# Kernel optimization log

Hardware: AMD Instinct MI355X
Metric: run time of the kernel (lower is better)

Reference implementation:

```python
import jax, jax.numpy as jnp
import numpy as np

N = 100000      # num graph nodes
E = 1600000     # num edges (avg degree 16)
IN = 128        # in_channels
H = 128         # hidden_channels
B = 4096        # query batch
CTX = 20        # context set length (indices[:, 3:])


def setup_inputs() -> dict:
    key = jax.random.key(0)
    ks = jax.random.split(key, 16)
    inp = {
        "indices": jax.random.randint(ks[0], (B, 3 + CTX), 0, N, dtype=jnp.int64),
        "src": jax.random.randint(ks[1], (E,), 0, N, dtype=jnp.int32),
        "dst": jax.random.randint(ks[2], (E,), 0, N, dtype=jnp.int32),
        "w": jax.random.uniform(ks[3], (E,), dtype=jnp.float32),
        # learned params
        "ndata": jax.random.normal(ks[4], (N, IN), dtype=jnp.float32),
        "W1": jax.random.normal(ks[5], (H, IN), dtype=jnp.float32) * (1.0 / np.sqrt(IN)),
        "b1": jnp.zeros((H,), jnp.float32),
        "W2": jax.random.normal(ks[6], (H, H), dtype=jnp.float32) * (1.0 / np.sqrt(H)),
        "b2": jnp.zeros((H,), jnp.float32),
        "eps": jnp.zeros((2,), jnp.float32),  # learn_eps, one per GINConv
        "Wc1": jax.random.normal(ks[7], (H, 3 * H), dtype=jnp.float32) * (1.0 / np.sqrt(3 * H)),
        "bc1": jnp.zeros((H,), jnp.float32),
        "Wc2": jax.random.normal(ks[8], (H // 2, H), dtype=jnp.float32) * (1.0 / np.sqrt(H)),
        "bc2": jnp.zeros((H // 2,), jnp.float32),
        "Wc3": jax.random.normal(ks[9], (1, H // 2), dtype=jnp.float32) * (1.0 / np.sqrt(H // 2)),
        "bc3": jnp.zeros((1,), jnp.float32),
    }
    return inp


def _gin_conv(x, src, dst, w, deg, eps, W, b):
    # DGL GINConv(mean, learn_eps): h = lin((1+eps)*x + mean_{in-edges}(w_e * x_src))
    msg = w[:, None] * x[src]                                   # [E, D]
    agg = jax.ops.segment_sum(msg, dst, num_segments=N) / deg   # [N, D]
    return ((1.0 + eps) * x + agg) @ W.T + b


def reference(indices, src, dst, w, ndata, W1, b1, W2, b2, eps,
              Wc1, bc1, Wc2, bc2, Wc3, bc3):
    deg = jax.ops.segment_sum(jnp.ones((E,), ndata.dtype), dst, num_segments=N)
    deg = jnp.maximum(deg, 1.0)[:, None]

    x = ndata
    x = jax.nn.relu(_gin_conv(x, src, dst, w, deg, eps[0], W1, b1))  # dropout inactive (eval)
    x = _gin_conv(x, src, dst, w, deg, eps[1], W2, b2)               # last layer: no relu
    x = x.at[0].set(0.0)                                             # x[0] = zeros

    ing1 = x[indices[:, 0]]   # [B, H]
    ing2 = x[indices[:, 1]]   # [B, H]

    # embed_context: mean over nonzero-index context members
    ctx_idx = indices[:, 3:]                                   # [B, CTX]
    ctx_sum = x[ctx_idx].sum(axis=1)                           # [B, H]
    norm = jnp.maximum((ctx_idx > 0).sum(axis=1), 1).astype(x.dtype)[:, None]
    ctx = ctx_sum / norm

    y = jnp.concatenate([ing1, ing2, ctx], axis=1)             # [B, 3H]
    y = jax.nn.relu(y @ Wc1.T + bc1)
    y = jax.nn.relu(y @ Wc2.T + bc2)
    y = y @ Wc3.T + bc3                                        # [B, 1]
    return y
```

## Files before the change

kernel.cpp:

```cpp
#include <hip/hip_runtime.h>


#define CONV_NPB 32
#define FIN_EPB 8

__global__ void init_kernel(const float* __restrict__ W1, const float* __restrict__ W2,
                            const float* __restrict__ Wc1, const float* __restrict__ Wc2,
                            float* __restrict__ Wt1, float* __restrict__ Wt2,
                            float* __restrict__ Wc1t, float* __restrict__ Wc2t,
                            int* __restrict__ cnt, int n) {
  int i = blockIdx.x * blockDim.x + threadIdx.x;
  if (i < n) cnt[i] = 0;
  if (i < 16384) {
    int f = i >> 7, k = i & 127;
    Wt1[k * 128 + f] = W1[i];
  } else if (i < 32768) {
    int j = i - 16384; int f = j >> 7, k = j & 127;
    Wt2[k * 128 + f] = W2[j];
  } else if (i < 81920) {
    int j = i - 32768; int f = j / 384, k = j % 384;
    Wc1t[k * 128 + f] = Wc1[j];
  } else if (i < 90112) {
    int j = i - 81920; int f = j >> 7, k = j & 127;
    Wc2t[k * 64 + f] = Wc2[j];
  }
}

__global__ void hist_kernel(const int* __restrict__ dst, int* __restrict__ cnt,
                            int* __restrict__ rank, int E) {
  int e = (blockIdx.x * blockDim.x + threadIdx.x) * 4;
  if (e + 3 < E) {
    const int4 d = *(const int4*)&dst[e];
    int4 r;
    r.x = atomicAdd(&cnt[d.x], 1);
    r.y = atomicAdd(&cnt[d.y], 1);
    r.z = atomicAdd(&cnt[d.z], 1);
    r.w = atomicAdd(&cnt[d.w], 1);
    *(int4*)&rank[e] = r;
  } else {
    for (; e < E; ++e) rank[e] = atomicAdd(&cnt[dst[e]], 1);
  }
}

__global__ void scan1_kernel(const int* __restrict__ cnt, int* __restrict__ prow,
                             int* __restrict__ bsum, int n) {
  __shared__ int smem[256];
  const int t = threadIdx.x;
  const int base = blockIdx.x * 2048 + t * 8;
  int v[8];
  int s = 0;
#pragma unroll
  for (int j = 0; j < 8; ++j) {
    int idx = base + j;
    v[j] = (idx < n) ? ((cnt[idx] + 7) & ~7) : 0;
    s += v[j];
  }
  smem[t] = s;
  __syncthreads();
  for (int off = 1; off < 256; off <<= 1) {
    int add = (t >= off) ? smem[t - off] : 0;
    __syncthreads();
    smem[t] += add;
    __syncthreads();
  }
  int run = smem[t] - s;
  if (t == 255) bsum[blockIdx.x] = smem[255];
#pragma unroll
  for (int j = 0; j < 8; ++j) {
    int idx = base + j;
    if (idx < n) prow[idx] = run;
    run += v[j];
  }
}

__global__ void scan2_kernel(int* __restrict__ bsum, int nb) {
  const int t = threadIdx.x;
  if (nb <= 64) {
    const int orig = (t < nb) ? bsum[t] : 0;
    int v = orig;
#pragma unroll
    for (int off = 1; off < 64; off <<= 1) {
      int u = __shfl_up(v, off);
      if (t >= off) v += u;
    }
    if (t == nb - 1) bsum[nb] = v;
    if (t < nb) bsum[t] = v - orig;
  } else if (t == 0) {
    int run = 0;
    for (int i = 0; i < nb; ++i) { int v = bsum[i]; bsum[i] = run; run += v; }
    bsum[nb] = run;
  }
}

__global__ void scatter_kernel(const int* __restrict__ src, const int* __restrict__ dst,
                               const float* __restrict__ w, const int* __restrict__ prow,
                               const int* __restrict__ bsum, const int* __restrict__ rank,
                               const int* __restrict__ cnt,
                               int2* __restrict__ epack, int E, int n) {
  const int i = blockIdx.x * blockDim.x + threadIdx.x;
  int e = i * 4;
  if (e + 3 < E) {
    const int4 d = *(const int4*)&dst[e];
    const int4 s = *(const int4*)&src[e];
    const float4 wv = *(const float4*)&w[e];
    const int4 r = *(const int4*)&rank[e];
    epack[prow[d.x] + bsum[d.x >> 11] + r.x] = make_int2(s.x, __float_as_int(wv.x));
    epack[prow[d.y] + bsum[d.y >> 11] + r.y] = make_int2(s.y, __float_as_int(wv.y));
    epack[prow[d.z] + bsum[d.z >> 11] + r.z] = make_int2(s.z, __float_as_int(wv.z));
    epack[prow[d.w] + bsum[d.w >> 11] + r.w] = make_int2(s.w, __float_as_int(wv.w));
  } else {
    for (; e < E; ++e) {
      const int d = dst[e];
      epack[prow[d] + bsum[d >> 11] + rank[e]] = make_int2(src[e], __float_as_int(w[e]));
    }
  }
  if (i < n) {
    const int c = cnt[i];
    const int start = prow[i] + bsum[i >> 11] + c;
    const int pc = ((c + 7) & ~7) - c;
    for (int j = 0; j < pc; ++j) epack[start + j] = make_int2(0, 0);
  }
}

__launch_bounds__(256, 6)
__global__ void conv_kernel(const float* __restrict__ xin, float* __restrict__ xout,
                            const int* __restrict__ prow, const int* __restrict__ bsum,
                            const int* __restrict__ cnt,
                            const int2* __restrict__ epack,
                            const float* __restrict__ Wt,
                            const float* __restrict__ bias, const float* __restrict__ eps,
                            int epsidx, int dorelu, int zerorow0, int n, int nchunk) {
  __shared__ float xm[CONV_NPB * 128];
  __shared__ int rp_s[CONV_NPB + 1];
  const int t = threadIdx.x;
  const int nb = blockIdx.x * CONV_NPB;
  const float epsv = 1.0f + eps[epsidx];

#pragma unroll
  for (int i = 0; i < 4; ++i)
    *(float4*)&xm[(t + i * 256) * 4] = make_float4(0.f, 0.f, 0.f, 0.f);
  if (t <= CONV_NPB) {
    const int node = nb + t;
    rp_s[t] = (node >= n) ? bsum[nchunk] : (prow[node] + bsum[node >> 11]);
  }
  __syncthreads();

  {
    const int L = t >> 5;
    const int lane = t & 31;
    const int f0 = lane * 4;
    const int e0 = rp_s[0], eT = rp_s[CONV_NPB];
    const int nbat = (eT - e0) >> 3;
    const int chunk = (((nbat + 7) >> 3)) << 3;
    const int jb = e0 + L * chunk;
    const int je = min(jb + chunk, eT);
    if (jb < je) {
      const int4* ep4 = (const int4*)epack;
      int r = 0;
      while (rp_s[r + 1] <= jb) ++r;
      float4 acc = make_float4(0.f, 0.f, 0.f, 0.f);
      for (int j = jb; j < je; j += 8) {
        if (rp_s[r + 1] <= j) {
          float* bp = &xm[r * 128 + lane];
          atomicAdd(bp + 0,  acc.x);
          atomicAdd(bp + 32, acc.y);
          atomicAdd(bp + 64, acc.z);
          atomicAdd(bp + 96, acc.w);
          acc = make_float4(0.f, 0.f, 0.f, 0.f);
          do { ++r; } while (rp_s[r + 1] <= j);
        }
        const int h = j >> 1;
        const int4 q0 = ep4[h + 0];
        const int4 q1 = ep4[h + 1];
        const int4 q2 = ep4[h + 2];
        const int4 q3 = ep4[h + 3];
        const float4 a0 = *(const float4*)&xin[(size_t)q0.x * 128 + f0];
        const float4 a1 = *(const float4*)&xin[(size_t)q0.z * 128 + f0];
        const float4 a2 = *(const float4*)&xin[(size_t)q1.x * 128 + f0];
        const float4 a3 = *(const float4*)&xin[(size_t)q1.z * 128 + f0];
        const float4 a4 = *(const float4*)&xin[(size_t)q2.x * 128 + f0];
        const float4 a5 = *(const float4*)&xin[(size_t)q2.z * 128 + f0];
        const float4 a6 = *(const float4*)&xin[(size_t)q3.x * 128 + f0];
        const float4 a7 = *(const float4*)&xin[(size_t)q3.z * 128 + f0];
        const float w0 = __int_as_float(q0.y), w1 = __int_as_float(q0.w);
        const float w2 = __int_as_float(q1.y), w3 = __int_as_float(q1.w);
        const float w4 = __int_as_float(q2.y), w5 = __int_as_float(q2.w);
        const float w6 = __int_as_float(q3.y), w7 = __int_as_float(q3.w);
        acc.x += w0 * a0.x + w1 * a1.x + w2 * a2.x + w3 * a3.x
               + w4 * a4.x + w5 * a5.x + w6 * a6.x + w7 * a7.x;
        acc.y += w0 * a0.y + w1 * a1.y + w2 * a2.y + w3 * a3.y
               + w4 * a4.y + w5 * a5.y + w6 * a6.y + w7 * a7.y;
        acc.z += w0 * a0.z + w1 * a1.z + w2 * a2.z + w3 * a3.z
               + w4 * a4.z + w5 * a5.z + w6 * a6.z + w7 * a7.z;
        acc.w += w0 * a0.w + w1 * a1.w + w2 * a2.w + w3 * a3.w
               + w4 * a4.w + w5 * a5.w + w6 * a6.w + w7 * a7.w;
      }
      float* bp = &xm[r * 128 + lane];
      atomicAdd(bp + 0,  acc.x);
      atomicAdd(bp + 32, acc.y);
      atomicAdd(bp + 64, acc.z);
      atomicAdd(bp + 96, acc.w);
    }
  }
  __syncthreads();

  {
    float4 m[4];
#pragma unroll
    for (int q = 0; q < 4; ++q) {
      const int task = t + q * 256;
      const int r = task >> 5;
      const int fg = task & 31;
      m[q].x = xm[r * 128 + fg];
      m[q].y = xm[r * 128 + 32 + fg];
      m[q].z = xm[r * 128 + 64 + fg];
      m[q].w = xm[r * 128 + 96 + fg];
    }
    __syncthreads();
#pragma unroll
    for (int q = 0; q < 4; ++q) {
      const int task = t + q * 256;
      const int r = task >> 5;
      const int fg = task & 31;
      const int f0 = fg * 4;
      const int node = nb + r;
      float4 v = make_float4(0.f, 0.f, 0.f, 0.f);
      if (node < n) {
        const int d = cnt[node];
        const float rdeg = 1.0f / (float)(d > 1 ? d : 1);
        const float4 xv = *(const float4*)&xin[(size_t)node * 128 + f0];
        v.x = epsv * xv.x + m[q].x * rdeg;
        v.y = epsv * xv.y + m[q].y * rdeg;
        v.z = epsv * xv.z + m[q].z * rdeg;
        v.w = epsv * xv.w + m[q].w * rdeg;
      }
      *(float4*)&xm[r * 128 + f0] = v;
    }
  }
  __syncthreads();

  {
    const int fg = t & 31;
    const int rg = t >> 5;
    const int f0 = fg * 4;
    const int r0 = rg * 4;
    float4 acc[4];
#pragma unroll
    for (int r = 0; r < 4; ++r) acc[r] = make_float4(0.f, 0.f, 0.f, 0.f);
    for (int k = 0; k < 128; k += 4) {
      const float4 w0 = *(const float4*)&Wt[(k + 0) * 128 + f0];
      const float4 w1 = *(const float4*)&Wt[(k + 1) * 128 + f0];
      const float4 w2 = *(const float4*)&Wt[(k + 2) * 128 + f0];
      const float4 w3 = *(const float4*)&Wt[(k + 3) * 128 + f0];
#pragma unroll
      for (int r = 0; r < 4; ++r) {
        const float4 xv = *(const float4*)&xm[(r0 + r) * 128 + k];
        acc[r].x += xv.x * w0.x + xv.y * w1.x + xv.z * w2.x + xv.w * w3.x;
        acc[r].y += xv.x * w0.y + xv.y * w1.y + xv.z * w2.y + xv.w * w3.y;
        acc[r].z += xv.x * w0.z + xv.y * w1.z + xv.z * w2.z + xv.w * w3.z;
        acc[r].w += xv.x * w0.w + xv.y * w1.w + xv.z * w2.w + xv.w * w3.w;
      }
    }
    const float4 bv = *(const float4*)&bias[f0];
#pragma unroll
    for (int r = 0; r < 4; ++r) {
      const int node = nb + r0 + r;
      if (node < n) {
        float4 v;
        v.x = acc[r].x + bv.x;
        v.y = acc[r].y + bv.y;
        v.z = acc[r].z + bv.z;
        v.w = acc[r].w + bv.w;
        if (dorelu) {
          v.x = fmaxf(v.x, 0.f); v.y = fmaxf(v.y, 0.f);
          v.z = fmaxf(v.z, 0.f); v.w = fmaxf(v.w, 0.f);
        }
        if (zerorow0 && node == 0) { v.x = 0.f; v.y = 0.f; v.z = 0.f; v.w = 0.f; }
        *(float4*)&xout[(size_t)node * 128 + f0] = v;
      }
    }
  }
}

__launch_bounds__(256, 4)
__global__ void final_kernel(const float* __restrict__ x2, const int* __restrict__ indices,
                             const float* __restrict__ Wc1t, const float* __restrict__ bc1,
                             const float* __restrict__ Wc2t, const float* __restrict__ bc2,
                             const float* __restrict__ Wc3, const float* __restrict__ bc3,
                             float* __restrict__ out) {
  __shared__ float ysm[FIN_EPB * 384];
  __shared__ float h1s[FIN_EPB * 128];
  __shared__ float h2s[FIN_EPB * 64];
  __shared__ int ind_s[FIN_EPB * 23];
  __shared__ float ccs[FIN_EPB];
  const int t = threadIdx.x;
  const int b0 = blockIdx.x * FIN_EPB;

  if (t < FIN_EPB * 23) ind_s[t] = indices[(size_t)b0 * 23 + t];
  __syncthreads();
  if (t < FIN_EPB) {
    int cc = 0;
#pragma unroll
    for (int j = 0; j < 20; ++j) cc += (ind_s[t * 23 + 3 + j] > 0) ? 1 : 0;
    ccs[t] = 1.0f / (float)(cc > 0 ? cc : 1);
  }
  __syncthreads();

  {
#pragma unroll
    for (int q = 0; q < 2; ++q) {
      const int s = t + q * 256;
      const int e = s >> 6;
      const int half = (s >> 5) & 1;
      const int fg = s & 31;
      const int idx = ind_s[e * 23 + half];
      *(float4*)&ysm[e * 384 + half * 128 + fg * 4] =
          *(const float4*)&x2[(size_t)idx * 128 + fg * 4];
    }
    const int e = t >> 5;
    const int fg = t & 31;
    float4 acc = make_float4(0.f, 0.f, 0.f, 0.f);
#pragma unroll
    for (int j = 0; j < 20; ++j) {
      const int cj = ind_s[e * 23 + 3 + j];
      const float4 a = *(const float4*)&x2[(size_t)cj * 128 + fg * 4];
      acc.x += a.x; acc.y += a.y; acc.z += a.z; acc.w += a.w;
    }
    const float sc = ccs[e];
    acc.x *= sc; acc.y *= sc; acc.z *= sc; acc.w *= sc;
    *(float4*)&ysm[e * 384 + 256 + fg * 4] = acc;
  }
  __syncthreads();

  {
    const int f1 = t & 127;
    const int eh = t >> 7;
    float acc[4];
    const float b = bc1[f1];
#pragma unroll
    for (int i = 0; i < 4; ++i) acc[i] = b;
    for (int k = 0; k < 384; k += 4) {
      const float wv0 = Wc1t[(k + 0) * 128 + f1];
      const float wv1 = Wc1t[(k + 1) * 128 + f1];
      const float wv2 = Wc1t[(k + 2) * 128 + f1];
      const float wv3 = Wc1t[(k + 3) * 128 + f1];
#pragma unroll
      for (int i = 0; i < 4; ++i) {
        const float4 yv = *(const float4*)&ysm[(eh * 4 + i) * 384 + k];
        acc[i] += yv.x * wv0 + yv.y * wv1 + yv.z * wv2 + yv.w * wv3;
      }
    }
#pragma unroll
    for (int i = 0; i < 4; ++i)
      h1s[(eh * 4 + i) * 128 + f1] = fmaxf(acc[i], 0.f);
  }
  __syncthreads();

  {
    const int f2 = t & 63;
    const int eg = t >> 6;
    float acc[2];
    const float b = bc2[f2];
#pragma unroll
    for (int i = 0; i < 2; ++i) acc[i] = b;
    for (int k = 0; k < 128; k += 4) {
      const float wv0 = Wc2t[(k + 0) * 64 + f2];
      const float wv1 = Wc2t[(k + 1) * 64 + f2];
      const float wv2 = Wc2t[(k + 2) * 64 + f2];
      const float wv3 = Wc2t[(k + 3) * 64 + f2];
#pragma unroll
      for (int i = 0; i < 2; ++i) {
        const float4 hv = *(const float4*)&h1s[(eg * 2 + i) * 128 + k];
        acc[i] += hv.x * wv0 + hv.y * wv1 + hv.z * wv2 + hv.w * wv3;
      }
    }
#pragma unroll
    for (int i = 0; i < 2; ++i)
      h2s[(eg * 2 + i) * 64 + f2] = fmaxf(acc[i], 0.f);
  }
  __syncthreads();

  {
    const int e = t >> 5;
    const int l = t & 31;
    float p = h2s[e * 64 + l] * Wc3[l] + h2s[e * 64 + l + 32] * Wc3[l + 32];
#pragma unroll
    for (int o = 16; o > 0; o >>= 1) p += __shfl_down(p, o, 32);
    if (l == 0) out[b0 + e] = p + bc3[0];
  }
}

extern "C" void kernel_launch(void* const* d_in, const int* in_sizes, int n_in,
                              void* d_out, int out_size, void* d_ws, size_t ws_size,
                              hipStream_t stream) {
  const int* indices = (const int*)d_in[0];
  const int* src = (const int*)d_in[1];
  const int* dst = (const int*)d_in[2];
  const float* w = (const float*)d_in[3];
  const float* ndata = (const float*)d_in[4];
  const float* W1 = (const float*)d_in[5];
  const float* b1 = (const float*)d_in[6];
  const float* W2 = (const float*)d_in[7];
  const float* b2 = (const float*)d_in[8];
  const float* eps = (const float*)d_in[9];
  const float* Wc1 = (const float*)d_in[10];
  const float* bc1 = (const float*)d_in[11];
  const float* Wc2 = (const float*)d_in[12];
  const float* bc2 = (const float*)d_in[13];
  const float* Wc3 = (const float*)d_in[14];
  const float* bc3 = (const float*)d_in[15];
  float* out = (float*)d_out;

  const int E = in_sizes[1];
  const int N = in_sizes[4] / 128;
  const int B = in_sizes[0] / 23;

  char* ws = (char*)d_ws;
  size_t off = 0;
  auto alloc = [&](size_t bytes) -> char* {
    char* p = ws + off;
    off = (off + bytes + 255) & ~(size_t)255;
    return p;
  };
  const size_t Epad = (size_t)E + 8 * (size_t)N;
  int* cnt = (int*)alloc((size_t)N * 4);
  int* prow = (int*)alloc((size_t)(N + 1) * 4);
  int* rank = (int*)alloc((size_t)E * 4);
  int* bsum = (int*)alloc(256 * 4);
  int2* epack = (int2*)alloc(Epad * 8);
  float* x1 = (float*)alloc((size_t)N * 128 * 4);
  float* x2 = (float*)alloc((size_t)N * 128 * 4);
  float* Wt1 = (float*)alloc(16384 * 4);
  float* Wt2 = (float*)alloc(16384 * 4);
  float* Wc1t = (float*)alloc(49152 * 4);
  float* Wc2t = (float*)alloc(8192 * 4);

  const int ninit = (N > 90112) ? N : 90112;
  init_kernel<<<(ninit + 255) / 256, 256, 0, stream>>>(W1, W2, Wc1, Wc2, Wt1, Wt2, Wc1t, Wc2t, cnt, N);
  const int Eq = (E + 3) / 4;
  hist_kernel<<<(Eq + 255) / 256, 256, 0, stream>>>(dst, cnt, rank, E);
  const int nchunk = (N + 2047) / 2048;
  scan1_kernel<<<nchunk, 256, 0, stream>>>(cnt, prow, bsum, N);
  scan2_kernel<<<1, 64, 0, stream>>>(bsum, nchunk);
  const int nsc = (Eq > N) ? Eq : N;
  scatter_kernel<<<(nsc + 255) / 256, 256, 0, stream>>>(src, dst, w, prow, bsum, rank, cnt, epack, E, N);

  const int nconv = (N + CONV_NPB - 1) / CONV_NPB;
  conv_kernel<<<nconv, 256, 0, stream>>>(ndata, x1, prow, bsum, cnt, epack, Wt1, b1, eps, 0, 1, 0, N, nchunk);
  conv_kernel<<<nconv, 256, 0, stream>>>(x1, x2, prow, bsum, cnt, epack, Wt2, b2, eps, 1, 0, 1, N, nchunk);

  final_kernel<<<B / FIN_EPB, 256, 0, stream>>>(x2, indices, Wc1t, bc1, Wc2t, bc2, Wc3, bc3, out);
}
```

Before: 593.0 us.

## Split fused conv into feature-sliced aggregation kernel and separate GEMM kernel

```diff
diff --git a/kernel.cpp b/kernel.cpp
--- a/kernel.cpp
+++ b/kernel.cpp
@@ -122,23 +122,22 @@
   }
 }
 
-__launch_bounds__(256, 6)
-__global__ void conv_kernel(const float* __restrict__ xin, float* __restrict__ xout,
-                            const int* __restrict__ prow, const int* __restrict__ bsum,
-                            const int* __restrict__ cnt,
-                            const int2* __restrict__ epack,
-                            const float* __restrict__ Wt,
-                            const float* __restrict__ bias, const float* __restrict__ eps,
-                            int epsidx, int dorelu, int zerorow0, int n, int nchunk) {
-  __shared__ float xm[CONV_NPB * 128];
+__launch_bounds__(256, 8)
+__global__ void agg_kernel(const float* __restrict__ xin, float* __restrict__ aggout,
+                           const int* __restrict__ prow, const int* __restrict__ bsum,
+                           const int2* __restrict__ epack,
+                           int n, int nchunk, int NB) {
+  __shared__ float xm[CONV_NPB * 32];
   __shared__ int rp_s[CONV_NPB + 1];
   const int t = threadIdx.x;
-  const int nb = blockIdx.x * CONV_NPB;
-  const float epsv = 1.0f + eps[epsidx];
-
-#pragma unroll
-  for (int i = 0; i < 4; ++i)
-    *(float4*)&xm[(t + i * 256) * 4] = make_float4(0.f, 0.f, 0.f, 0.f);
+  const int bid = blockIdx.x;
+  const int x8 = bid & 7;
+  const int q = x8 >> 1;
+  const int nb0 = ((bid >> 3) << 1) + (x8 & 1);
+  if (nb0 >= NB) return;
+  const int nb = nb0 * CONV_NPB;
+
+  *(float4*)&xm[t * 4] = make_float4(0.f, 0.f, 0.f, 0.f);
   if (t <= CONV_NPB) {
     const int node = nb + t;
     rp_s[t] = (node >= n) ? bsum[nchunk] : (prow[node] + bsum[node >> 11]);
@@ -148,7 +147,9 @@
   {
     const int L = t >> 5;
     const int lane = t & 31;
-    const int f0 = lane * 4;
+    const int fg = lane & 7;
+    const int ksl = lane >> 3;
+    const int f0 = q * 32 + fg * 4;
     const int e0 = rp_s[0], eT = rp_s[CONV_NPB];
     const int nbat = (eT - e0) >> 3;
     const int chunk = (((nbat + 7) >> 3)) << 3;
@@ -161,81 +162,74 @@
       float4 acc = make_float4(0.f, 0.f, 0.f, 0.f);
       for (int j = jb; j < je; j += 8) {
         if (rp_s[r + 1] <= j) {
-          float* bp = &xm[r * 128 + lane];
+          float* bp = &xm[r * 32 + fg];
           atomicAdd(bp + 0,  acc.x);
-          atomicAdd(bp + 32, acc.y);
-          atomicAdd(bp + 64, acc.z);
-          atomicAdd(bp + 96, acc.w);
+          atomicAdd(bp + 8,  acc.y);
+          atomicAdd(bp + 16, acc.z);
+          atomicAdd(bp + 24, acc.w);
           acc = make_float4(0.f, 0.f, 0.f, 0.f);
           do { ++r; } while (rp_s[r + 1] <= j);
         }
         const int h = j >> 1;
-        const int4 q0 = ep4[h + 0];
-        const int4 q1 = ep4[h + 1];
-        const int4 q2 = ep4[h + 2];
-        const int4 q3 = ep4[h + 3];
-        const float4 a0 = *(const float4*)&xin[(size_t)q0.x * 128 + f0];
-        const float4 a1 = *(const float4*)&xin[(size_t)q0.z * 128 + f0];
-        const float4 a2 = *(const float4*)&xin[(size_t)q1.x * 128 + f0];
-        const float4 a3 = *(const float4*)&xin[(size_t)q1.z * 128 + f0];
-        const float4 a4 = *(const float4*)&xin[(size_t)q2.x * 128 + f0];
-        const float4 a5 = *(const float4*)&xin[(size_t)q2.z * 128 + f0];
-        const float4 a6 = *(const float4*)&xin[(size_t)q3.x * 128 + f0];
-        const float4 a7 = *(const float4*)&xin[(size_t)q3.z * 128 + f0];
-        const float w0 = __int_as_float(q0.y), w1 = __int_as_float(q0.w);
-        const float w2 = __int_as_float(q1.y), w3 = __int_as_float(q1.w);
-        const float w4 = __int_as_float(q2.y), w5 = __int_as_float(q2.w);
-        const float w6 = __int_as_float(q3.y), w7 = __int_as_float(q3.w);
-        acc.x += w0 * a0.x + w1 * a1.x + w2 * a2.x + w3 * a3.x
-               + w4 * a4.x + w5 * a5.x + w6 * a6.x + w7 * a7.x;
-        acc.y += w0 * a0.y + w1 * a1.y + w2 * a2.y + w3 * a3.y
-               + w4 * a4.y + w5 * a5.y + w6 * a6.y + w7 * a7.y;
-        acc.z += w0 * a0.z + w1 * a1.z + w2 * a2.z + w3 * a3.z
-               + w4 * a4.z + w5 * a5.z + w6 * a6.z + w7 * a7.z;
-        acc.w += w0 * a0.w + w1 * a1.w + w2 * a2.w + w3 * a3.w
-               + w4 * a4.w + w5 * a5.w + w6 * a6.w + w7 * a7.w;
+        const int4 d = ep4[h + ksl];
+        const float4 a0 = *(const float4*)&xin[(size_t)d.x * 128 + f0];
+        const float4 a1 = *(const float4*)&xin[(size_t)d.z * 128 + f0];
+        const float w0 = __int_as_float(d.y), w1 = __int_as_float(d.w);
+        acc.x += w0 * a0.x + w1 * a1.x;
+        acc.y += w0 * a0.y + w1 * a1.y;
+        acc.z += w0 * a0.z + w1 * a1.z;
+        acc.w += w0 * a0.w + w1 * a1.w;
       }
-      float* bp = &xm[r * 128 + lane];
+      float* bp = &xm[r * 32 + fg];
       atomicAdd(bp + 0,  acc.x);
-      atomicAdd(bp + 32, acc.y);
-      atomicAdd(bp + 64, acc.z);
-      atomicAdd(bp + 96, acc.w);
-    }
-  }
-  __syncthreads();
-
-  {
-    float4 m[4];
-#pragma unroll
-    for (int q = 0; q < 4; ++q) {
-      const int task = t + q * 256;
-      const int r = task >> 5;
-      const int fg = task & 31;
-      m[q].x = xm[r * 128 + fg];
-      m[q].y = xm[r * 128 + 32 + fg];
-      m[q].z = xm[r * 128 + 64 + fg];
-      m[q].w = xm[r * 128 + 96 + fg];
-    }
-    __syncthreads();
-#pragma unroll
-    for (int q = 0; q < 4; ++q) {
-      const int task = t + q * 256;
-      const int r = task >> 5;
-      const int fg = task & 31;
-      const int f0 = fg * 4;
-      const int node = nb + r;
-      float4 v = make_float4(0.f, 0.f, 0.f, 0.f);
-      if (node < n) {
-        const int d = cnt[node];
-        const float rdeg = 1.0f / (float)(d > 1 ? d : 1);
-        const float4 xv = *(const float4*)&xin[(size_t)node * 128 + f0];
-        v.x = epsv * xv.x + m[q].x * rdeg;
-        v.y = epsv * xv.y + m[q].y * rdeg;
-        v.z = epsv * xv.z + m[q].z * rdeg;
-        v.w = epsv * xv.w + m[q].w * rdeg;
-      }
-      *(float4*)&xm[r * 128 + f0] = v;
-    }
+      atomicAdd(bp + 8,  acc.y);
+      atomicAdd(bp + 16, acc.z);
+      atomicAdd(bp + 24, acc.w);
+    }
+  }
+  __syncthreads();
+
+#pragma unroll
+  for (int k = 0; k < 4; ++k) {
+    const int task = t + k * 256;
+    const int r = task >> 5;
+    const int f = task & 31;
+    const int node = nb + r;
+    if (node < n)
+      aggout[(size_t)node * 128 + q * 32 + f] = xm[r * 32 + (f & 3) * 8 + (f >> 2)];
+  }
+}
+
+__launch_bounds__(256, 6)
+__global__ void gemm_kernel(const float* __restrict__ xin, const float* agg,
+                            float* xout, const int* __restrict__ cnt,
+                            const float* __restrict__ Wt, const float* __restrict__ bias,
+                            const float* __restrict__ eps, int epsidx, int dorelu,
+                            int zerorow0, int n) {
+  __shared__ float xm[CONV_NPB * 128];
+  const int t = threadIdx.x;
+  const int nb = blockIdx.x * CONV_NPB;
+  const float epsv = 1.0f + eps[epsidx];
+
+#pragma unroll
+  for (int kq = 0; kq < 4; ++kq) {
+    const int task = t + kq * 256;
+    const int r = task >> 5;
+    const int fg = task & 31;
+    const int f0 = fg * 4;
+    const int node = nb + r;
+    float4 v = make_float4(0.f, 0.f, 0.f, 0.f);
+    if (node < n) {
+      const int d = cnt[node];
+      const float rdeg = 1.0f / (float)(d > 1 ? d : 1);
+      const float4 xv = *(const float4*)&xin[(size_t)node * 128 + f0];
+      const float4 av = *(const float4*)&agg[(size_t)node * 128 + f0];
+      v.x = epsv * xv.x + av.x * rdeg;
+      v.y = epsv * xv.y + av.y * rdeg;
+      v.z = epsv * xv.z + av.z * rdeg;
+      v.w = epsv * xv.w + av.w * rdeg;
+    }
+    *(float4*)&xm[r * 128 + f0] = v;
   }
   __syncthreads();
 
@@ -445,9 +439,13 @@
   const int nsc = (Eq > N) ? Eq : N;
   scatter_kernel<<<(nsc + 255) / 256, 256, 0, stream>>>(src, dst, w, prow, bsum, rank, cnt, epack, E, N);
 
-  const int nconv = (N + CONV_NPB - 1) / CONV_NPB;
-  conv_kernel<<<nconv, 256, 0, stream>>>(ndata, x1, prow, bsum, cnt, epack, Wt1, b1, eps, 0, 1, 0, N, nchunk);
-  conv_kernel<<<nconv, 256, 0, stream>>>(x1, x2, prow, bsum, cnt, epack, Wt2, b2, eps, 1, 0, 1, N, nchunk);
+  const int NB = (N + CONV_NPB - 1) / CONV_NPB;
+  const int gridA = 8 * ((NB + 1) / 2);
+
+  agg_kernel<<<gridA, 256, 0, stream>>>(ndata, x2, prow, bsum, epack, N, nchunk, NB);
+  gemm_kernel<<<NB, 256, 0, stream>>>(ndata, x2, x1, cnt, Wt1, b1, eps, 0, 1, 0, N);
+  agg_kernel<<<gridA, 256, 0, stream>>>(x1, x2, prow, bsum, epack, N, nchunk, NB);
+  gemm_kernel<<<NB, 256, 0, stream>>>(x1, x2, x2, cnt, Wt2, b2, eps, 1, 0, 1, N);
 
   final_kernel<<<B / FIN_EPB, 256, 0, stream>>>(x2, indices, Wc1t, bc1, Wc2t, bc2, Wc3, bc3, out);
 }
```

Measured after the change: 1.026 ms. +73.1%, slower.
